# Optimization experiments

Measured on AMD Instinct MI355X. Metric: run time of the kernel, lower is better.

The kernel has to match this reference:

```python
import jax, jax.numpy as jnp
import numpy as np

NHEAD = 16
HEAD_DIM = 64
ROPE_BASE = 10000.0


def _rotate_half(x):
    # interleaved convention: pairs (x0,x1)->(-x1,x0)
    x1 = x[..., ::2]
    x2 = x[..., 1::2]
    return jnp.stack([-x2, x1], axis=-1).reshape(x.shape)


def _rope_cache(seq_len, head_dim, base):
    half = head_dim // 2
    inv_freq = 1.0 / base ** (jnp.arange(half, dtype=jnp.float32) / float(half))
    t = jnp.arange(seq_len, dtype=jnp.float32)
    freqs = jnp.einsum('i,j->ij', t, inv_freq)          # [T, half]
    emb = jnp.concatenate([freqs, freqs], axis=-1)      # [T, D] (half-half cat, matches torch source)
    return jnp.cos(emb), jnp.sin(emb)


def setup_inputs() -> dict:
    key = jax.random.key(0)
    k1, k2, k3 = jax.random.split(key, 3)
    b, t, c = 2, 2048, 1024
    x = jax.random.normal(k1, (b, t, c), dtype=jnp.float32)
    # torch nn.Linear weights: [out_features, in_features], scaled like kaiming-uniform-ish
    W_qkv = jax.random.normal(k2, (3 * c, c), dtype=jnp.float32) / np.sqrt(c)
    W_out = jax.random.normal(k3, (c, c), dtype=jnp.float32) / np.sqrt(c)
    return {"x": x, "W_qkv": W_qkv, "W_out": W_out}


def reference(x, W_qkv, W_out):
    b, t, c = x.shape
    nh, hd = NHEAD, HEAD_DIM
    qkv = x @ W_qkv.T                                   # [b, t, 3c]
    q, k, v = jnp.split(qkv, 3, axis=-1)

    def to_heads(a):
        return a.reshape(b, t, nh, hd).transpose(0, 2, 1, 3)  # [b, nh, t, hd]

    q, k, v = to_heads(q), to_heads(k), to_heads(v)
    cos, sin = _rope_cache(t, hd, ROPE_BASE)            # [t, hd]
    cos = cos.astype(q.dtype)[None, None]
    sin = sin.astype(q.dtype)[None, None]
    q = q * cos + _rotate_half(q) * sin
    k = k * cos + _rotate_half(k) * sin

    scale = 1.0 / np.sqrt(hd).astype(np.float32)
    scores = jnp.einsum('bhqd,bhkd->bhqk', q, k) * scale
    attn = jax.nn.softmax(scores, axis=-1)
    y = jnp.einsum('bhqk,bhkd->bhqd', attn, v)          # [b, nh, t, hd]
    y = y.transpose(0, 2, 1, 3).reshape(b, t, c)
    return y @ W_out.T
```

## Files before the change

kernel.cpp:

```cpp
#include <hip/hip_runtime.h>
#include <hip/hip_bf16.h>
#include <math.h>

typedef __hip_bfloat16 bf16;
typedef _Float16 f16;
typedef __attribute__((ext_vector_type(8))) short bf16x8;
typedef __attribute__((ext_vector_type(8))) _Float16 f16x8;
typedef __attribute__((ext_vector_type(4))) float f32x4;
typedef __attribute__((ext_vector_type(4))) unsigned u32x4;

#define MFMA_BF(a,b,c) __builtin_amdgcn_mfma_f32_16x16x32_bf16((a),(b),(c),0,0,0)
#define MFMA_F16(a,b,c) __builtin_amdgcn_mfma_f32_16x16x32_f16((a),(b),(c),0,0,0)

__device__ __forceinline__ void load_lds16(const void* g, void* l) {
  __builtin_amdgcn_global_load_lds(
      (__attribute__((address_space(1))) void*)(g),
      (__attribute__((address_space(3))) void*)(l), 16, 0, 0);
}

__device__ __forceinline__ unsigned pk_bf16(float a, float b) {
  unsigned ua = __builtin_bit_cast(unsigned, a);
  unsigned ub = __builtin_bit_cast(unsigned, b);
  ua += 0x7fffu + ((ua >> 16) & 1u);
  ub += 0x7fffu + ((ub >> 16) & 1u);
  return (ua >> 16) | (ub & 0xffff0000u);
}

__global__ void cvt_all(const float* __restrict__ x, const float* __restrict__ wq,
                        const float* __restrict__ wo, unsigned* __restrict__ xb,
                        unsigned* __restrict__ wqb, unsigned* __restrict__ wob) {
  int i = blockIdx.x * blockDim.x + threadIdx.x;
  const float* src;
  unsigned* dst;
  int off;
  if (i < 1048576) { src = x; dst = xb; off = i; }
  else if (i < 1048576 + 786432) { src = wq; dst = wqb; off = i - 1048576; }
  else { src = wo; dst = wob; off = i - (1048576 + 786432); }
  float4 v = reinterpret_cast<const float4*>(src)[off];
  uint2 u;
  u.x = pk_bf16(v.x, v.y);
  u.y = pk_bf16(v.z, v.w);
  reinterpret_cast<uint2*>(dst)[off] = u;
}

__global__ __launch_bounds__(256, 2)
void gemm_qkv(const bf16* __restrict__ A, const bf16* __restrict__ B,
              bf16* __restrict__ outq, bf16* __restrict__ outk,
              f16* __restrict__ outv) {
  __shared__ __align__(16) bf16 As[3][128 * 32];
  __shared__ __align__(16) bf16 Bs[3][128 * 32];
  const int K = 1024;
  const int tid = threadIdx.x;
  const int w = tid >> 6;
  const int lane = tid & 63;
  const int quad = lane >> 4;
  const int col = lane & 15;
  const int waveM = w >> 1;
  const int waveN = w & 1;
  const int bm = blockIdx.y * 128;
  const int bn = blockIdx.x * 128;

  f32x4 acc[4][4] = {};
  const int srow = lane >> 2;
  const int skoff = (((lane & 3) ^ ((srow >> 1) & 3))) * 8;
  const int swq = (quad ^ ((col >> 1) & 3)) * 8;

  auto stage = [&](int k0, int sb) {
#pragma unroll
    for (int p = 0; p < 2; ++p) {
      int r = p * 64 + w * 16 + srow;
      load_lds16(A + (size_t)(bm + r) * K + k0 + skoff,
                 (char*)As + sb * 8192 + p * 4096 + w * 1024);
      load_lds16(B + (size_t)(bn + r) * K + k0 + skoff,
                 (char*)Bs + sb * 8192 + p * 4096 + w * 1024);
    }
  };

  stage(0, 0);
  stage(32, 1);

  int cb = 0;
  for (int k0 = 0; k0 < K; k0 += 32) {
    if (k0 + 32 < K) __asm__ volatile("s_waitcnt vmcnt(4)" ::: "memory");
    else             __asm__ volatile("s_waitcnt vmcnt(0)" ::: "memory");
    __asm__ volatile("s_barrier" ::: "memory");
    if (k0 + 64 < K) {
      int nb = cb + 2; if (nb >= 3) nb -= 3;
      stage(k0 + 64, nb);
    }
    const bf16* at = &As[cb][0];
    const bf16* bt = &Bs[cb][0];
    bf16x8 af[4], bfr[4];
#pragma unroll
    for (int i = 0; i < 4; ++i)
      af[i] = *reinterpret_cast<const bf16x8*>(at + (waveM * 64 + i * 16 + col) * 32 + swq);
#pragma unroll
    for (int j = 0; j < 4; ++j)
      bfr[j] = *reinterpret_cast<const bf16x8*>(bt + (waveN * 64 + j * 16 + col) * 32 + swq);
#pragma unroll
    for (int i = 0; i < 4; ++i)
#pragma unroll
      for (int j = 0; j < 4; ++j)
        acc[i][j] = MFMA_BF(af[i], bfr[j], acc[i][j]);
    cb = (cb == 2) ? 0 : cb + 1;
  }

  if (bn < 2048) {
    const float NEGK = -0.4152410118f;
    const float C1 = 0.1803368799f;
    const float sgn = (col & 1) ? 1.0f : -1.0f;
#pragma unroll
    for (int j = 0; j < 4; ++j) {
      const int n0 = bn + waveN * 64 + j * 16;
      const int sel = n0 >> 10;
      const int hh = (n0 & 1023) >> 6;
      const int dd = (n0 & 63) + col;
      bf16* outp = sel ? outk : outq;
      const float post = sel ? 1.0f : C1;
      const float invf = __builtin_amdgcn_exp2f((float)((n0 & 31) + col) * NEGK);
#pragma unroll
      for (int i = 0; i < 4; ++i) {
#pragma unroll
        for (int r = 0; r < 4; ++r) {
          int m = bm + waveM * 64 + i * 16 + quad * 4 + r;
          int b = m >> 11, t = m & 2047;
          float v = acc[i][j][r];
          float partner = __shfl_xor(v, 1);
          float ang = (float)t * invf;
          float res = (v * __cosf(ang) + sgn * partner * __sinf(ang)) * post;
          outp[((size_t)(b * 16 + hh) * 2048 + t) * 64 + dd] = __float2bfloat16(res);
        }
      }
    }
  } else {
    const int b = bm >> 11;
    const int tt0 = (bm & 2047) + waveM * 64;
#pragma unroll
    for (int j = 0; j < 4; ++j) {
      const int n0 = bn + waveN * 64 + j * 16;
      const int hh = (n0 & 1023) >> 6;
      const int dd = (n0 & 63) + col;
      f16* dst = outv + (size_t)(b * 16 + hh) * 131072 + (size_t)dd * 2048;
#pragma unroll
      for (int i = 0; i < 4; ++i) {
        uint2 pk;
        pk.x = __builtin_bit_cast(unsigned, __builtin_amdgcn_cvt_pkrtz(acc[i][j][0], acc[i][j][1]));
        pk.y = __builtin_bit_cast(unsigned, __builtin_amdgcn_cvt_pkrtz(acc[i][j][2], acc[i][j][3]));
        *reinterpret_cast<uint2*>(dst + tt0 + i * 16 + quad * 4) = pk;
      }
    }
  }
}

__global__ __launch_bounds__(256, 2)
void gemm_out(const bf16* __restrict__ A, const bf16* __restrict__ B,
              float* __restrict__ outf) {
  __shared__ __align__(16) bf16 As[3][64 * 32];
  __shared__ __align__(16) bf16 Bs[3][128 * 32];
  const int K = 1024;
  const int tid = threadIdx.x;
  const int w = tid >> 6;
  const int lane = tid & 63;
  const int quad = lane >> 4;
  const int col = lane & 15;
  const int bm = blockIdx.y * 64;
  const int bn = blockIdx.x * 128;

  f32x4 acc[4][2] = {};
  const int srow = lane >> 2;
  const int skoff = (((lane & 3) ^ ((srow >> 1) & 3))) * 8;
  const int swq = (quad ^ ((col >> 1) & 3)) * 8;

  auto stage = [&](int k0, int sb) {
    load_lds16(A + (size_t)(bm + w * 16 + srow) * K + k0 + skoff,
               (char*)As + sb * 4096 + w * 1024);
#pragma unroll
    for (int p = 0; p < 2; ++p)
      load_lds16(B + (size_t)(bn + p * 64 + w * 16 + srow) * K + k0 + skoff,
                 (char*)Bs + sb * 8192 + p * 4096 + w * 1024);
  };

  stage(0, 0);
  stage(32, 1);

  int cb = 0;
  for (int k0 = 0; k0 < K; k0 += 32) {
    if (k0 + 32 < K) __asm__ volatile("s_waitcnt vmcnt(3)" ::: "memory");
    else             __asm__ volatile("s_waitcnt vmcnt(0)" ::: "memory");
    __asm__ volatile("s_barrier" ::: "memory");
    if (k0 + 64 < K) {
      int nb = cb + 2; if (nb >= 3) nb -= 3;
      stage(k0 + 64, nb);
    }
    const bf16* at = &As[cb][0];
    const bf16* bt = &Bs[cb][0];
    bf16x8 af[4], bfr[2];
#pragma unroll
    for (int i = 0; i < 4; ++i)
      af[i] = *reinterpret_cast<const bf16x8*>(at + (i * 16 + col) * 32 + swq);
#pragma unroll
    for (int j = 0; j < 2; ++j)
      bfr[j] = *reinterpret_cast<const bf16x8*>(bt + (w * 32 + j * 16 + col) * 32 + swq);
#pragma unroll
    for (int i = 0; i < 4; ++i)
#pragma unroll
      for (int j = 0; j < 2; ++j)
        acc[i][j] = MFMA_BF(af[i], bfr[j], acc[i][j]);
    cb = (cb == 2) ? 0 : cb + 1;
  }

#pragma unroll
  for (int i = 0; i < 4; ++i)
#pragma unroll
    for (int j = 0; j < 2; ++j) {
      const int n0 = bn + w * 32 + j * 16;
#pragma unroll
      for (int r = 0; r < 4; ++r) {
        int m = bm + i * 16 + quad * 4 + r;
        outf[(size_t)m * 1024 + n0 + col] = acc[i][j][r];
      }
    }
}

__global__ __launch_bounds__(256, 3)
void attn_kernel(const bf16* __restrict__ qh, const bf16* __restrict__ kh,
                 const f16* __restrict__ vt, bf16* __restrict__ y) {
  __shared__ __align__(16) bf16 Ks[3][64 * 64];
  __shared__ __align__(16) f16 Vs[3][64 * 64];

  const int bh = blockIdx.y;
  const int w = threadIdx.x >> 6;
  const int lane = threadIdx.x & 63;
  const int quad = lane >> 4;
  const int col = lane & 15;

  const int qrow0 = blockIdx.x * 128 + w * 32 + col;
  bf16x8 qf[2][2];
#pragma unroll
  for (int f = 0; f < 2; ++f)
#pragma unroll
    for (int c = 0; c < 2; ++c)
      qf[f][c] = *reinterpret_cast<const bf16x8*>(
          qh + ((size_t)bh * 2048 + qrow0 + f * 16) * 64 + c * 32 + quad * 8);

  const int s8 = lane >> 3;
  const int blk = (lane & 7) ^ s8;
  const bf16* kg = kh + (size_t)bh * 2048 * 64;
  const f16* vg = vt + (size_t)bh * 64 * 2048;
  const int ks0 = 32 * (w >> 1) + 8 * ((4 * w + (s8 >> 2)) & 3) + 4 * (w & 1) + (s8 & 3);
  const int ks1 = 32 * (w >> 1) + 8 * ((4 * w + 2 + (s8 >> 2)) & 3) + 4 * (w & 1) + (s8 & 3);
  const int vrow0 = w * 16 + s8;

  const int csw = col & 7;
  const int sw0 = (quad ^ csw) * 8;
  const int sw1 = ((quad + 4) ^ csw) * 8;
  const int rdbase = col * 64;

  f32x4 O[2][4] = {};
  float l[2] = {};

  auto stage = [&](int kn, int sb) {
    char* kb = (char*)Ks + sb * 8192 + w * 2048;
    char* vb = (char*)Vs + sb * 8192 + w * 2048;
    load_lds16(kg + (size_t)(kn + ks0) * 64 + blk * 8, kb);
    load_lds16(kg + (size_t)(kn + ks1) * 64 + blk * 8, kb + 1024);
    load_lds16(vg + (size_t)vrow0 * 2048 + kn + blk * 8, vb);
    load_lds16(vg + (size_t)(vrow0 + 8) * 2048 + kn + blk * 8, vb + 1024);
  };

  stage(0, 0);
  stage(64, 1);

  int cb = 0;
  for (int kc = 0; kc < 2048; kc += 64) {
    if (kc + 64 < 2048) __asm__ volatile("s_waitcnt vmcnt(4)" ::: "memory");
    else                __asm__ volatile("s_waitcnt vmcnt(0)" ::: "memory");
    __asm__ volatile("s_barrier" ::: "memory");
    if (kc + 128 < 2048) {
      int nb = cb + 2; if (nb >= 3) nb -= 3;
      stage(kc + 128, nb);
    }

    const bf16* kt = &Ks[cb][0];
    const f16* vtile = &Vs[cb][0];

    f32x4 s[2][4];
#pragma unroll
    for (int t = 0; t < 4; ++t) {
      bf16x8 kf0 = *reinterpret_cast<const bf16x8*>(kt + t * 1024 + rdbase + sw0);
      bf16x8 kf1 = *reinterpret_cast<const bf16x8*>(kt + t * 1024 + rdbase + sw1);
#pragma unroll
      for (int f = 0; f < 2; ++f) {
        f32x4 a = {};
        a = MFMA_BF(kf0, qf[f][0], a);
        a = MFMA_BF(kf1, qf[f][1], a);
        s[f][t] = a;
      }
    }

    f16x8 pf[2][2];
#pragma unroll
    for (int f = 0; f < 2; ++f) {
      unsigned pk[8];
      float lf = 0.0f;
#pragma unroll
      for (int t = 0; t < 4; ++t) {
        float p0 = __builtin_amdgcn_exp2f(s[f][t][0]);
        float p1 = __builtin_amdgcn_exp2f(s[f][t][1]);
        float p2 = __builtin_amdgcn_exp2f(s[f][t][2]);
        float p3 = __builtin_amdgcn_exp2f(s[f][t][3]);
        lf += (p0 + p1) + (p2 + p3);
        pk[t * 2]     = __builtin_bit_cast(unsigned, __builtin_amdgcn_cvt_pkrtz(p0, p1));
        pk[t * 2 + 1] = __builtin_bit_cast(unsigned, __builtin_amdgcn_cvt_pkrtz(p2, p3));
      }
      l[f] += lf;
      pf[f][0] = __builtin_bit_cast(f16x8, (u32x4){pk[0], pk[1], pk[2], pk[3]});
      pf[f][1] = __builtin_bit_cast(f16x8, (u32x4){pk[4], pk[5], pk[6], pk[7]});
    }

#pragma unroll
    for (int j = 0; j < 4; ++j) {
      f16x8 vf0 = *reinterpret_cast<const f16x8*>(vtile + j * 1024 + rdbase + sw0);
      f16x8 vf1 = *reinterpret_cast<const f16x8*>(vtile + j * 1024 + rdbase + sw1);
#pragma unroll
      for (int f = 0; f < 2; ++f) {
        O[f][j] = MFMA_F16(vf0, pf[f][0], O[f][j]);
        O[f][j] = MFMA_F16(vf1, pf[f][1], O[f][j]);
      }
    }
    cb = (cb == 2) ? 0 : cb + 1;
  }

  const int b = bh >> 4, h = bh & 15;
#pragma unroll
  for (int f = 0; f < 2; ++f) {
    float lv = l[f];
    lv += __shfl_xor(lv, 16, 64);
    lv += __shfl_xor(lv, 32, 64);
    float inv = 1.0f / lv;
    int tq = blockIdx.x * 128 + w * 32 + f * 16 + col;
    size_t base = ((size_t)b * 2048 + tq) * 1024 + h * 64;
#pragma unroll
    for (int j = 0; j < 4; ++j) {
      uint2 pk2;
      pk2.x = pk_bf16(O[f][j][0] * inv, O[f][j][1] * inv);
      pk2.y = pk_bf16(O[f][j][2] * inv, O[f][j][3] * inv);
      *reinterpret_cast<uint2*>((unsigned short*)y + base + j * 16 + quad * 4) = pk2;
    }
  }
}

extern "C" void kernel_launch(void* const* d_in, const int* in_sizes, int n_in,
                              void* d_out, int out_size, void* d_ws, size_t ws_size,
                              hipStream_t stream) {
  const float* x    = (const float*)d_in[0];
  const float* wqkv = (const float*)d_in[1];
  const float* wout = (const float*)d_in[2];
  float* out = (float*)d_out;
  char* ws = (char*)d_ws;

  bf16* xb    = (bf16*)(ws);
  bf16* wqkvb = (bf16*)(ws + (size_t)(8 << 20));
  bf16* woutb = (bf16*)(ws + (size_t)(14 << 20));
  bf16* qh    = (bf16*)(ws + (size_t)(16 << 20));
  bf16* kh    = (bf16*)(ws + (size_t)(24 << 20));
  f16*  vt    = (f16*) (ws + (size_t)(32 << 20));
  bf16* y     = (bf16*)(ws + (size_t)(40 << 20));

  cvt_all<<<8192, 256, 0, stream>>>(x, wqkv, wout,
                                    (unsigned*)xb, (unsigned*)wqkvb, (unsigned*)woutb);
  gemm_qkv<<<dim3(24, 32), 256, 0, stream>>>(xb, wqkvb, qh, kh, vt);
  attn_kernel<<<dim3(16, 32), 256, 0, stream>>>(qh, kh, vt, y);
  gemm_out<<<dim3(8, 64), 256, 0, stream>>>(y, woutb, out);
}
```

Before: 178.0 us.

## Split attention KV tile across warp pairs with LDS reduction of partial outputs

Restructures the attention kernel so each pair of warps shares 64 query rows and each warp processes half of every 64-key tile. This makes each warp reuse K/V fragments across four query subtiles instead of two, cutting LDS reads per MFMA. The partial O and row sums are combined through LDS at the end. It doubles per-warp accumulator registers, so occupancy drops to 2 blocks per launch bound and the kernel gains an extra sync and reduction step.

New measurement: 178.8 us. About the same (+0.5%).

```diff
diff --git a/kernel.cpp b/kernel.cpp
--- a/kernel.cpp
+++ b/kernel.cpp
@@ -222,7 +222,7 @@
     }
 }
 
-__global__ __launch_bounds__(256, 3)
+__global__ __launch_bounds__(256, 2)
 void attn_kernel(const bf16* __restrict__ qh, const bf16* __restrict__ kh,
                  const f16* __restrict__ vt, bf16* __restrict__ y) {
   __shared__ __align__(16) bf16 Ks[3][64 * 64];
@@ -233,39 +233,42 @@
   const int lane = threadIdx.x & 63;
   const int quad = lane >> 4;
   const int col = lane & 15;
-
-  const int qrow0 = blockIdx.x * 128 + w * 32 + col;
-  bf16x8 qf[2][2];
-#pragma unroll
-  for (int f = 0; f < 2; ++f)
+  const int kg = w & 1;
+  const int qg = w >> 1;
+
+  const int qbase = blockIdx.x * 128 + qg * 64 + col;
+  bf16x8 qf[4][2];
+#pragma unroll
+  for (int f = 0; f < 4; ++f)
 #pragma unroll
     for (int c = 0; c < 2; ++c)
       qf[f][c] = *reinterpret_cast<const bf16x8*>(
-          qh + ((size_t)bh * 2048 + qrow0 + f * 16) * 64 + c * 32 + quad * 8);
+          qh + ((size_t)bh * 2048 + qbase + f * 16) * 64 + c * 32 + quad * 8);
 
   const int s8 = lane >> 3;
   const int blk = (lane & 7) ^ s8;
-  const bf16* kg = kh + (size_t)bh * 2048 * 64;
-  const f16* vg = vt + (size_t)bh * 64 * 2048;
-  const int ks0 = 32 * (w >> 1) + 8 * ((4 * w + (s8 >> 2)) & 3) + 4 * (w & 1) + (s8 & 3);
-  const int ks1 = 32 * (w >> 1) + 8 * ((4 * w + 2 + (s8 >> 2)) & 3) + 4 * (w & 1) + (s8 & 3);
+  const bf16* kg_ptr = kh + (size_t)bh * 2048 * 64;
+  const f16* vg_ptr = vt + (size_t)bh * 64 * 2048;
+  const int ks0 = (w >> 1) * 32 + (w & 1) * 4 + 8 * (s8 >> 2) + (s8 & 3);
+  const int ks1 = ks0 + 16;
   const int vrow0 = w * 16 + s8;
 
   const int csw = col & 7;
   const int sw0 = (quad ^ csw) * 8;
   const int sw1 = ((quad + 4) ^ csw) * 8;
-  const int rdbase = col * 64;
-
-  f32x4 O[2][4] = {};
-  float l[2] = {};
+  const int vsw = ((kg * 4 + quad) ^ csw) * 8;
+  const int krow = kg * 32;
+
+  f32x4 O[4][4] = {};
+  float l[4] = {};
 
   auto stage = [&](int kn, int sb) {
     char* kb = (char*)Ks + sb * 8192 + w * 2048;
     char* vb = (char*)Vs + sb * 8192 + w * 2048;
-    load_lds16(kg + (size_t)(kn + ks0) * 64 + blk * 8, kb);
-    load_lds16(kg + (size_t)(kn + ks1) * 64 + blk * 8, kb + 1024);
-    load_lds16(vg + (size_t)vrow0 * 2048 + kn + blk * 8, vb);
-    load_lds16(vg + (size_t)(vrow0 + 8) * 2048 + kn + blk * 8, vb + 1024);
+    load_lds16(kg_ptr + (size_t)(kn + ks0) * 64 + blk * 8, kb);
+    load_lds16(kg_ptr + (size_t)(kn + ks1) * 64 + blk * 8, kb + 1024);
+    load_lds16(vg_ptr + (size_t)vrow0 * 2048 + kn + blk * 8, vb);
+    load_lds16(vg_ptr + (size_t)(vrow0 + 8) * 2048 + kn + blk * 8, vb + 1024);
   };
 
   stage(0, 0);
@@ -281,71 +284,92 @@
       stage(kc + 128, nb);
     }
 
-    const bf16* kt = &Ks[cb][0];
+    const bf16* kt_p = &Ks[cb][0];
     const f16* vtile = &Vs[cb][0];
 
+    bf16x8 kf[2][2];
+#pragma unroll
+    for (int t = 0; t < 2; ++t) {
+      kf[t][0] = *reinterpret_cast<const bf16x8*>(kt_p + (krow + t * 16 + col) * 64 + sw0);
+      kf[t][1] = *reinterpret_cast<const bf16x8*>(kt_p + (krow + t * 16 + col) * 64 + sw1);
+    }
+
     f32x4 s[2][4];
 #pragma unroll
-    for (int t = 0; t < 4; ++t) {
-      bf16x8 kf0 = *reinterpret_cast<const bf16x8*>(kt + t * 1024 + rdbase + sw0);
-      bf16x8 kf1 = *reinterpret_cast<const bf16x8*>(kt + t * 1024 + rdbase + sw1);
-#pragma unroll
-      for (int f = 0; f < 2; ++f) {
+    for (int t = 0; t < 2; ++t)
+#pragma unroll
+      for (int f = 0; f < 4; ++f) {
         f32x4 a = {};
-        a = MFMA_BF(kf0, qf[f][0], a);
-        a = MFMA_BF(kf1, qf[f][1], a);
-        s[f][t] = a;
-      }
-    }
-
-    f16x8 pf[2][2];
-#pragma unroll
-    for (int f = 0; f < 2; ++f) {
-      unsigned pk[8];
-      float lf = 0.0f;
-#pragma unroll
-      for (int t = 0; t < 4; ++t) {
-        float p0 = __builtin_amdgcn_exp2f(s[f][t][0]);
-        float p1 = __builtin_amdgcn_exp2f(s[f][t][1]);
-        float p2 = __builtin_amdgcn_exp2f(s[f][t][2]);
-        float p3 = __builtin_amdgcn_exp2f(s[f][t][3]);
-        lf += (p0 + p1) + (p2 + p3);
-        pk[t * 2]     = __builtin_bit_cast(unsigned, __builtin_amdgcn_cvt_pkrtz(p0, p1));
-        pk[t * 2 + 1] = __builtin_bit_cast(unsigned, __builtin_amdgcn_cvt_pkrtz(p2, p3));
-      }
-      l[f] += lf;
-      pf[f][0] = __builtin_bit_cast(f16x8, (u32x4){pk[0], pk[1], pk[2], pk[3]});
-      pf[f][1] = __builtin_bit_cast(f16x8, (u32x4){pk[4], pk[5], pk[6], pk[7]});
-    }
-
-#pragma unroll
-    for (int j = 0; j < 4; ++j) {
-      f16x8 vf0 = *reinterpret_cast<const f16x8*>(vtile + j * 1024 + rdbase + sw0);
-      f16x8 vf1 = *reinterpret_cast<const f16x8*>(vtile + j * 1024 + rdbase + sw1);
-#pragma unroll
-      for (int f = 0; f < 2; ++f) {
-        O[f][j] = MFMA_F16(vf0, pf[f][0], O[f][j]);
-        O[f][j] = MFMA_F16(vf1, pf[f][1], O[f][j]);
-      }
+        a = MFMA_BF(kf[t][0], qf[f][0], a);
+        a = MFMA_BF(kf[t][1], qf[f][1], a);
+        s[t][f] = a;
+      }
+
+    f16x8 pf[4];
+#pragma unroll
+    for (int f = 0; f < 4; ++f) {
+      float p00 = __builtin_amdgcn_exp2f(s[0][f][0]);
+      float p01 = __builtin_amdgcn_exp2f(s[0][f][1]);
+      float p02 = __builtin_amdgcn_exp2f(s[0][f][2]);
+      float p03 = __builtin_amdgcn_exp2f(s[0][f][3]);
+      float p10 = __builtin_amdgcn_exp2f(s[1][f][0]);
+      float p11 = __builtin_amdgcn_exp2f(s[1][f][1]);
+      float p12 = __builtin_amdgcn_exp2f(s[1][f][2]);
+      float p13 = __builtin_amdgcn_exp2f(s[1][f][3]);
+      l[f] += ((p00 + p01) + (p02 + p03)) + ((p10 + p11) + (p12 + p13));
+      u32x4 pk;
+      pk.x = __builtin_bit_cast(unsigned, __builtin_amdgcn_cvt_pkrtz(p00, p01));
+      pk.y = __builtin_bit_cast(unsigned, __builtin_amdgcn_cvt_pkrtz(p02, p03));
+      pk.z = __builtin_bit_cast(unsigned, __builtin_amdgcn_cvt_pkrtz(p10, p11));
+      pk.w = __builtin_bit_cast(unsigned, __builtin_amdgcn_cvt_pkrtz(p12, p13));
+      pf[f] = __builtin_bit_cast(f16x8, pk);
+    }
+
+#pragma unroll
+    for (int jt = 0; jt < 4; ++jt) {
+      f16x8 vf = *reinterpret_cast<const f16x8*>(vtile + (jt * 16 + col) * 64 + vsw);
+#pragma unroll
+      for (int f = 0; f < 4; ++f)
+        O[jt][f] = MFMA_F16(vf, pf[f], O[jt][f]);
     }
     cb = (cb == 2) ? 0 : cb + 1;
   }
 
-  const int b = bh >> 4, h = bh & 15;
-#pragma unroll
-  for (int f = 0; f < 2; ++f) {
-    float lv = l[f];
-    lv += __shfl_xor(lv, 16, 64);
-    lv += __shfl_xor(lv, 32, 64);
-    float inv = 1.0f / lv;
-    int tq = blockIdx.x * 128 + w * 32 + f * 16 + col;
-    size_t base = ((size_t)b * 2048 + tq) * 1024 + h * 64;
-#pragma unroll
-    for (int j = 0; j < 4; ++j) {
-      uint2 pk2;
-      pk2.x = pk_bf16(O[f][j][0] * inv, O[f][j][1] * inv);
-      pk2.y = pk_bf16(O[f][j][2] * inv, O[f][j][3] * inv);
-      *reinterpret_cast<uint2*>((unsigned short*)y + base + j * 16 + quad * 4) = pk2;
+#pragma unroll
+  for (int f = 0; f < 4; ++f) {
+    l[f] += __shfl_xor(l[f], 16, 64);
+    l[f] += __shfl_xor(l[f], 32, 64);
+  }
+
+  float* xb = (float*)&Ks[0][0];
+  if (kg == 1) {
+    float* dst = xb + qg * 4352 + lane * 68;
+#pragma unroll
+    for (int jt = 0; jt < 4; ++jt)
+#pragma unroll
+      for (int f = 0; f < 4; ++f)
+        *reinterpret_cast<f32x4*>(dst + (jt * 4 + f) * 4) = O[jt][f];
+#pragma unroll
+    for (int f = 0; f < 4; ++f) dst[64 + f] = l[f];
+  }
+  __syncthreads();
+  if (kg == 0) {
+    const float* src = xb + qg * 4352 + lane * 68;
+    const int b = bh >> 4, h = bh & 15;
+#pragma unroll
+    for (int f = 0; f < 4; ++f) {
+      float lv = l[f] + src[64 + f];
+      float inv = 1.0f / lv;
+      int q = qbase - col + f * 16 + col;
+      size_t base = ((size_t)b * 2048 + q) * 1024 + h * 64;
+#pragma unroll
+      for (int jt = 0; jt < 4; ++jt) {
+        f32x4 o = O[jt][f] + *reinterpret_cast<const f32x4*>(src + (jt * 4 + f) * 4);
+        uint2 pk2;
+        pk2.x = pk_bf16(o[0] * inv, o[1] * inv);
+        pk2.y = pk_bf16(o[2] * inv, o[3] * inv);
+        *reinterpret_cast<uint2*>((unsigned short*)y + base + jt * 16 + quad * 4) = pk2;
+      }
     }
   }
 }
```
